# Kernel optimization log

Hardware: AMD Instinct MI355X
Metric: run time of the kernel (lower is better)

Reference implementation:

```python
import jax, jax.numpy as jnp
import numpy as np

N = 8192
ALPHA = 0.1520  # curve_fit of 1/(1+a x^(2b)) to exp(-(x-min_dist)/spread), spread=5, min_dist=1e-5
BETA = 0.7900


def gcn_propagate(x, src, dst, dinv_sqrt):
    # symmetric-normalized aggregation with self loops: A_hat x
    norm = dinv_sqrt[src] * dinv_sqrt[dst]          # [E]
    msg = x[src] * norm[:, None]                     # [E, D]
    agg = jax.ops.segment_sum(msg, dst, num_segments=N)
    agg = agg + x * (dinv_sqrt * dinv_sqrt)[:, None]  # self-loop term x_i / deg_i
    return agg


def setup_inputs() -> dict:
    key = jax.random.key(0)
    k1, k2, k3, k4 = jax.random.split(key, 4)
    E = 262144
    features = jax.random.normal(k1, (N, 512), dtype=jnp.float32)
    edge_index = jax.random.randint(k2, (2, E), 0, N, dtype=jnp.int32)
    W1 = jax.random.normal(k3, (512, 256), dtype=jnp.float32) * 0.05
    b1 = jnp.zeros((256,), dtype=jnp.float32)
    W2 = jax.random.normal(k4, (256, 2), dtype=jnp.float32) * 0.05
    b2 = jnp.zeros((2,), dtype=jnp.float32)
    return {"features": features, "edge_index": edge_index,
            "W1": W1, "b1": b1, "W2": W2, "b2": b2}


def reference(features, edge_index, W1, b1, W2, b2):
    src, dst = edge_index[0], edge_index[1]
    # degree with self loops
    deg = jax.ops.segment_sum(jnp.ones_like(dst, dtype=jnp.float32), dst,
                              num_segments=N) + 1.0
    dinv_sqrt = 1.0 / jnp.sqrt(deg)
    # GCN: layer1 (relu) -> layer2 (linear), dropout_rate=0
    h = gcn_propagate(features, src, dst, dinv_sqrt) @ W1 + b1
    h = jax.nn.relu(h)
    emb = gcn_propagate(h, src, dst, dinv_sqrt) @ W2 + b2   # [N, 2]
    # pairwise squared euclidean distances (cdist^2)
    sq = jnp.sum(emb * emb, axis=1)                          # [N]
    d2 = jnp.maximum(sq[:, None] + sq[None, :] - 2.0 * (emb @ emb.T), 0.0)
    # q = 1 / (1 + alpha * d^(2*beta)) = 1 / (1 + alpha * (d^2)^beta)
    d2_safe = jnp.where(d2 > 0, d2, 1.0)
    pw = jnp.where(d2 > 0, jnp.power(d2_safe, BETA), 0.0)
    q = 1.0 / (1.0 + ALPHA * pw)
    return emb, q
```

## Files before the change

kernel.cpp:

```cpp
#include <hip/hip_runtime.h>
#include <math.h>

#define NN 8192
#define DD 512
#define HH 256
#define EE 262144
#define ALPHAC 0.1520f
#define BETAC  0.7900f

typedef float floatx4 __attribute__((ext_vector_type(4)));

__global__ __launch_bounds__(256) void zero_cnt_kernel(int* __restrict__ cnt) {
  cnt[blockIdx.x * 256 + threadIdx.x] = 0;
}

__global__ __launch_bounds__(256) void count_edges_kernel(const int* __restrict__ dst,
                                                          int* __restrict__ cnt) {
  int e = blockIdx.x * 256 + threadIdx.x;
  atomicAdd(&cnt[dst[e]], 1);
}

__global__ __launch_bounds__(256) void scan_build_kernel(const int* __restrict__ cnt,
    int* __restrict__ row_ptr, int* __restrict__ cursor, float* __restrict__ dinv) {
  int t = threadIdx.x;
  int base = t * 32;
  int local[32];
  int s = 0;
#pragma unroll
  for (int k = 0; k < 32; ++k) { local[k] = cnt[base + k]; s += local[k]; }
  int inc = s;
#pragma unroll
  for (int off = 1; off < 64; off <<= 1) {
    int v = __shfl_up(inc, off, 64);
    if ((t & 63) >= off) inc += v;
  }
  __shared__ int wsum[4];
  int lane = t & 63, wid = t >> 6;
  if (lane == 63) wsum[wid] = inc;
  __syncthreads();
  int woff = 0;
  for (int w = 0; w < wid; ++w) woff += wsum[w];
  int run = woff + inc - s;
#pragma unroll
  for (int k = 0; k < 32; ++k) {
    row_ptr[base + k] = run;
    cursor[base + k] = run;
    dinv[base + k] = rsqrtf((float)cnt[base + k] + 1.0f);
    run += local[k];
  }
  if (t == 255) row_ptr[NN] = run;
}

__global__ __launch_bounds__(256) void scatter_edges_kernel(const int* __restrict__ src,
    const int* __restrict__ dst, int* __restrict__ cursor,
    const float* __restrict__ dinv, int* __restrict__ srcs, float* __restrict__ norms) {
  int e = blockIdx.x * 256 + threadIdx.x;
  int s = src[e], d = dst[e];
  int pos = atomicAdd(&cursor[d], 1);
  srcs[pos] = s;
  norms[pos] = dinv[s];
}

#define BM 128
#define BN 64
#define BK 16
__global__ __launch_bounds__(256) void gemm1_kernel(const float* __restrict__ A,
    const float* __restrict__ B, float* __restrict__ C) {
  __shared__ float As[BK][BM + 4];
  __shared__ float Bs[BK][BN + 4];
  int t = threadIdx.x;
  int tx = t & 15;
  int ty = t >> 4;
  int m0 = blockIdx.y * BM, n0 = blockIdx.x * BN;
  int arow = t >> 1;
  int acol = (t & 1) * 8;
  int brow = t >> 4;
  int bcol = (t & 15) * 4;

  const float* aptr0 = &A[(size_t)(m0 + arow) * DD + acol];
  const float* bptr = &B[(size_t)brow * HH + n0 + bcol];

  float acc[8][4] = {};
  float4 a0v = *(const float4*)(aptr0 + 0);
  float4 a1v = *(const float4*)(aptr0 + 4);
  float4 bv = *(const float4*)(bptr);

  for (int k0 = 0; k0 < DD; k0 += BK) {
    As[acol + 0][arow] = a0v.x; As[acol + 1][arow] = a0v.y;
    As[acol + 2][arow] = a0v.z; As[acol + 3][arow] = a0v.w;
    As[acol + 4][arow] = a1v.x; As[acol + 5][arow] = a1v.y;
    As[acol + 6][arow] = a1v.z; As[acol + 7][arow] = a1v.w;
    *(float4*)&Bs[brow][bcol] = bv;
    __syncthreads();
    if (k0 + BK < DD) {
      a0v = *(const float4*)(aptr0 + k0 + BK + 0);
      a1v = *(const float4*)(aptr0 + k0 + BK + 4);
      bv = *(const float4*)(bptr + (size_t)(k0 + BK) * HH);
    }
#pragma unroll
    for (int k = 0; k < BK; ++k) {
      float4 xa = *(const float4*)&As[k][ty * 8];
      float4 xb = *(const float4*)&As[k][ty * 8 + 4];
      float4 bb = *(const float4*)&Bs[k][tx * 4];
      float am[8] = {xa.x, xa.y, xa.z, xa.w, xb.x, xb.y, xb.z, xb.w};
      float bn[4] = {bb.x, bb.y, bb.z, bb.w};
#pragma unroll
      for (int i = 0; i < 8; ++i)
#pragma unroll
        for (int j = 0; j < 4; ++j) acc[i][j] = fmaf(am[i], bn[j], acc[i][j]);
    }
    __syncthreads();
  }
#pragma unroll
  for (int i = 0; i < 8; ++i) {
    float4 o = make_float4(acc[i][0], acc[i][1], acc[i][2], acc[i][3]);
    *(float4*)&C[(size_t)(m0 + ty * 8 + i) * HH + n0 + tx * 4] = o;
  }
}

__global__ __launch_bounds__(256) void layer1_kernel(const float* __restrict__ t1,
    const int* __restrict__ row_ptr, const int* __restrict__ srcs,
    const float* __restrict__ norms, const float* __restrict__ dinv,
    const float* __restrict__ b1, const float* __restrict__ W2,
    float* __restrict__ t2) {
  int wid = threadIdx.x >> 6;
  int lane = threadIdx.x & 63;
  int i = blockIdx.x * 4 + wid;
  float di = dinv[i];
  int beg = row_ptr[i], end = row_ptr[i + 1];
  float4 acc = make_float4(0.f, 0.f, 0.f, 0.f);
  for (int base = beg; base < end; base += 64) {
    int cnt = end - base;
    if (cnt > 64) cnt = 64;
    int s_reg = 0;
    float n_reg = 0.f;
    if (lane < cnt) { s_reg = srcs[base + lane]; n_reg = norms[base + lane]; }
    int c = 0;
    for (; c + 4 <= cnt; c += 4) {
      int s0 = __shfl(s_reg, c, 64), s1 = __shfl(s_reg, c + 1, 64);
      int s2 = __shfl(s_reg, c + 2, 64), s3 = __shfl(s_reg, c + 3, 64);
      float q0 = __shfl(n_reg, c, 64), q1 = __shfl(n_reg, c + 1, 64);
      float q2 = __shfl(n_reg, c + 2, 64), q3 = __shfl(n_reg, c + 3, 64);
      float4 v0 = *(const float4*)&t1[(size_t)s0 * HH + lane * 4];
      float4 v1 = *(const float4*)&t1[(size_t)s1 * HH + lane * 4];
      float4 v2 = *(const float4*)&t1[(size_t)s2 * HH + lane * 4];
      float4 v3 = *(const float4*)&t1[(size_t)s3 * HH + lane * 4];
      acc.x = fmaf(q0, v0.x, fmaf(q1, v1.x, fmaf(q2, v2.x, fmaf(q3, v3.x, acc.x))));
      acc.y = fmaf(q0, v0.y, fmaf(q1, v1.y, fmaf(q2, v2.y, fmaf(q3, v3.y, acc.y))));
      acc.z = fmaf(q0, v0.z, fmaf(q1, v1.z, fmaf(q2, v2.z, fmaf(q3, v3.z, acc.z))));
      acc.w = fmaf(q0, v0.w, fmaf(q1, v1.w, fmaf(q2, v2.w, fmaf(q3, v3.w, acc.w))));
    }
    for (; c < cnt; ++c) {
      int s = __shfl(s_reg, c, 64);
      float qn = __shfl(n_reg, c, 64);
      float4 v = *(const float4*)&t1[(size_t)s * HH + lane * 4];
      acc.x = fmaf(qn, v.x, acc.x);
      acc.y = fmaf(qn, v.y, acc.y);
      acc.z = fmaf(qn, v.z, acc.z);
      acc.w = fmaf(qn, v.w, acc.w);
    }
  }
  float4 self = *(const float4*)&t1[(size_t)i * HH + lane * 4];
  float4 bv = *(const float4*)&b1[lane * 4];
  float dd = di * di;
  float4 h;
  h.x = fmaxf(fmaf(di, acc.x, fmaf(dd, self.x, bv.x)), 0.f);
  h.y = fmaxf(fmaf(di, acc.y, fmaf(dd, self.y, bv.y)), 0.f);
  h.z = fmaxf(fmaf(di, acc.z, fmaf(dd, self.z, bv.z)), 0.f);
  h.w = fmaxf(fmaf(di, acc.w, fmaf(dd, self.w, bv.w)), 0.f);
  float4 w0 = *(const float4*)&W2[lane * 8];
  float4 w1 = *(const float4*)&W2[lane * 8 + 4];
  float p0 = h.x * w0.x + h.y * w0.z + h.z * w1.x + h.w * w1.z;
  float p1 = h.x * w0.y + h.y * w0.w + h.z * w1.y + h.w * w1.w;
#pragma unroll
  for (int off = 32; off > 0; off >>= 1) {
    p0 += __shfl_down(p0, off, 64);
    p1 += __shfl_down(p1, off, 64);
  }
  if (lane == 0) {
    t2[i * 2 + 0] = p0;
    t2[i * 2 + 1] = p1;
  }
}

__global__ __launch_bounds__(256) void layer2_kernel(const float* __restrict__ t2,
    const int* __restrict__ row_ptr, const int* __restrict__ srcs,
    const float* __restrict__ norms, const float* __restrict__ dinv,
    const float* __restrict__ b2, float* __restrict__ emb, float* __restrict__ sq) {
  int wid = threadIdx.x >> 6;
  int lane = threadIdx.x & 63;
  int i = blockIdx.x * 4 + wid;
  float di = dinv[i];
  int beg = row_ptr[i], end = row_ptr[i + 1];
  float a0 = 0.f, a1 = 0.f;
  for (int e = beg + lane; e < end; e += 64) {
    int s = srcs[e];
    float ns = norms[e];
    a0 += ns * t2[2 * s + 0];
    a1 += ns * t2[2 * s + 1];
  }
#pragma unroll
  for (int off = 32; off > 0; off >>= 1) {
    a0 += __shfl_down(a0, off, 64);
    a1 += __shfl_down(a1, off, 64);
  }
  if (lane == 0) {
    float e0 = di * a0 + di * di * t2[2 * i + 0] + b2[0];
    float e1 = di * a1 + di * di * t2[2 * i + 1] + b2[1];
    emb[2 * i + 0] = e0;
    emb[2 * i + 1] = e1;
    sq[i] = e0 * e0 + e1 * e1;
  }
}

__global__ __launch_bounds__(256) void q_kernel(const float* __restrict__ emb,
    const float* __restrict__ sq, float* __restrict__ q) {
  int t = threadIdx.x;
  int j0 = blockIdx.x * 1024 + t * 4;
  int i0 = blockIdx.y * 32;
  float ex[4], ey[4], sj[4];
#pragma unroll
  for (int jj = 0; jj < 4; ++jj) {
    ex[jj] = emb[2 * (j0 + jj) + 0];
    ey[jj] = emb[2 * (j0 + jj) + 1];
    sj[jj] = sq[j0 + jj];
  }
  for (int ii = 0; ii < 32; ++ii) {
    int i = i0 + ii;
    float xi = emb[2 * i + 0], yi = emb[2 * i + 1], si = sq[i];
    float out4[4];
#pragma unroll
    for (int jj = 0; jj < 4; ++jj) {
      float d2 = si + sj[jj] - 2.f * (xi * ex[jj] + yi * ey[jj]);
      d2 = fmaxf(d2, 0.f);
      float pw = __expf(BETAC * __logf(d2));
      float den = fmaf(ALPHAC, pw, 1.f);
      float qv = __builtin_amdgcn_rcpf(den);
      out4[jj] = (d2 > 0.f) ? qv : 1.f;
    }
    floatx4 r = {out4[0], out4[1], out4[2], out4[3]};
    __builtin_nontemporal_store(r, (floatx4*)&q[(size_t)i * NN + j0]);
  }
}

extern "C" void kernel_launch(void* const* d_in, const int* in_sizes, int n_in,
                              void* d_out, int out_size, void* d_ws, size_t ws_size,
                              hipStream_t stream) {
  const float* features = (const float*)d_in[0];
  const int* edge_index = (const int*)d_in[1];
  const float* W1 = (const float*)d_in[2];
  const float* b1 = (const float*)d_in[3];
  const float* W2 = (const float*)d_in[4];
  const float* b2 = (const float*)d_in[5];
  float* out = (float*)d_out;

  const int* src = edge_index;
  const int* dst = edge_index + EE;

  int* cnt = (int*)d_ws;
  int* row_ptr = cnt + NN;
  int* cursor = row_ptr + 8448;
  int* srcs = cursor + NN;
  float* norms = (float*)(srcs + EE);
  float* dinv = norms + EE;
  float* sqv = dinv + NN;
  float* t2 = sqv + NN;
  float* t1 = t2 + 2 * NN;

  float* emb = out;
  float* qout = out + 2 * NN;

  zero_cnt_kernel<<<NN / 256, 256, 0, stream>>>(cnt);
  count_edges_kernel<<<EE / 256, 256, 0, stream>>>(dst, cnt);
  scan_build_kernel<<<1, 256, 0, stream>>>(cnt, row_ptr, cursor, dinv);
  scatter_edges_kernel<<<EE / 256, 256, 0, stream>>>(src, dst, cursor, dinv, srcs, norms);
  gemm1_kernel<<<dim3(HH / BN, NN / BM), 256, 0, stream>>>(features, W1, t1);
  layer1_kernel<<<NN / 4, 256, 0, stream>>>(t1, row_ptr, srcs, norms, dinv, b1, W2, t2);
  layer2_kernel<<<NN / 4, 256, 0, stream>>>(t2, row_ptr, srcs, norms, dinv, b2, emb, sqv);
  q_kernel<<<dim3(NN / 1024, NN / 32), 256, 0, stream>>>(emb, sqv, qout);
}
```

Measured before the change: 380.7 us.

## Use split-fp16 MFMA for the features×W1 GEMM instead of FP32 FMA

Rewrites gemm1 to split each fp32 input into a high fp16 part and a scaled low fp16 residual. It then runs three 16x16x32 f16 MFMA products per tile (hi*hi, hi*lo, lo*hi) to emulate near-fp32 accuracy on matrix cores. This targets the scalar FMA throughput limit of the old GEMM. The cost is conversion work, extra LDS traffic and 3x the MFMA count, plus a small precision loss from dropping the lo*lo term and fp16 range limits.

```diff
diff --git a/kernel.cpp b/kernel.cpp
--- a/kernel.cpp
+++ b/kernel.cpp
@@ -9,6 +9,8 @@
 #define BETAC  0.7900f
 
 typedef float floatx4 __attribute__((ext_vector_type(4)));
+typedef _Float16 half8 __attribute__((ext_vector_type(8)));
+typedef _Float16 half4 __attribute__((ext_vector_type(4)));
 
 __global__ __launch_bounds__(256) void zero_cnt_kernel(int* __restrict__ cnt) {
   cnt[blockIdx.x * 256 + threadIdx.x] = 0;
@@ -61,61 +63,106 @@
   norms[pos] = dinv[s];
 }
 
-#define BM 128
-#define BN 64
-#define BK 16
+#define LDAH 40
 __global__ __launch_bounds__(256) void gemm1_kernel(const float* __restrict__ A,
     const float* __restrict__ B, float* __restrict__ C) {
-  __shared__ float As[BK][BM + 4];
-  __shared__ float Bs[BK][BN + 4];
+  __shared__ __align__(16) _Float16 AsH[128 * LDAH];
+  __shared__ __align__(16) _Float16 AsL[128 * LDAH];
+  __shared__ __align__(16) _Float16 BtH[64 * LDAH];
+  __shared__ __align__(16) _Float16 BtL[64 * LDAH];
   int t = threadIdx.x;
-  int tx = t & 15;
-  int ty = t >> 4;
-  int m0 = blockIdx.y * BM, n0 = blockIdx.x * BN;
-  int arow = t >> 1;
-  int acol = (t & 1) * 8;
-  int brow = t >> 4;
-  int bcol = (t & 15) * 4;
-
-  const float* aptr0 = &A[(size_t)(m0 + arow) * DD + acol];
-  const float* bptr = &B[(size_t)brow * HH + n0 + bcol];
-
-  float acc[8][4] = {};
-  float4 a0v = *(const float4*)(aptr0 + 0);
-  float4 a1v = *(const float4*)(aptr0 + 4);
-  float4 bv = *(const float4*)(bptr);
-
-  for (int k0 = 0; k0 < DD; k0 += BK) {
-    As[acol + 0][arow] = a0v.x; As[acol + 1][arow] = a0v.y;
-    As[acol + 2][arow] = a0v.z; As[acol + 3][arow] = a0v.w;
-    As[acol + 4][arow] = a1v.x; As[acol + 5][arow] = a1v.y;
-    As[acol + 6][arow] = a1v.z; As[acol + 7][arow] = a1v.w;
-    *(float4*)&Bs[brow][bcol] = bv;
+  int wid = t >> 6, lane = t & 63;
+  int wr = wid >> 1, wc = wid & 1;
+  int m0 = blockIdx.y * 128, n0 = blockIdx.x * 64;
+  int fr = lane & 15;
+  int koff = (lane >> 4) * 8;
+  int bc = t & 63;
+  int bkr = (t >> 6) * 8;
+
+  floatx4 accH[4][2] = {};
+  floatx4 accC[4][2] = {};
+
+  const float* Abase = A + (size_t)m0 * DD;
+  float4 aReg[4];
+  float bReg[8];
+#pragma unroll
+  for (int i = 0; i < 4; ++i) {
+    int f = t + 256 * i;
+    aReg[i] = *(const float4*)&Abase[(size_t)(f >> 3) * DD + (f & 7) * 4];
+  }
+#pragma unroll
+  for (int j = 0; j < 8; ++j) bReg[j] = B[(size_t)(bkr + j) * HH + n0 + bc];
+
+  for (int k0 = 0; k0 < DD; k0 += 32) {
+#pragma unroll
+    for (int i = 0; i < 4; ++i) {
+      int f = t + 256 * i;
+      int row = f >> 3, c4 = f & 7;
+      float4 v = aReg[i];
+      half4 h, l;
+      h.x = (_Float16)v.x; l.x = (_Float16)((v.x - (float)h.x) * 2048.f);
+      h.y = (_Float16)v.y; l.y = (_Float16)((v.y - (float)h.y) * 2048.f);
+      h.z = (_Float16)v.z; l.z = (_Float16)((v.z - (float)h.z) * 2048.f);
+      h.w = (_Float16)v.w; l.w = (_Float16)((v.w - (float)h.w) * 2048.f);
+      *(half4*)&AsH[row * LDAH + c4 * 4] = h;
+      *(half4*)&AsL[row * LDAH + c4 * 4] = l;
+    }
+    {
+      half8 h, l;
+#pragma unroll
+      for (int j = 0; j < 8; ++j) {
+        float v = bReg[j];
+        _Float16 hh = (_Float16)v;
+        h[j] = hh;
+        l[j] = (_Float16)((v - (float)hh) * 2048.f);
+      }
+      *(half8*)&BtH[bc * LDAH + bkr] = h;
+      *(half8*)&BtL[bc * LDAH + bkr] = l;
+    }
     __syncthreads();
-    if (k0 + BK < DD) {
-      a0v = *(const float4*)(aptr0 + k0 + BK + 0);
-      a1v = *(const float4*)(aptr0 + k0 + BK + 4);
-      bv = *(const float4*)(bptr + (size_t)(k0 + BK) * HH);
-    }
-#pragma unroll
-    for (int k = 0; k < BK; ++k) {
-      float4 xa = *(const float4*)&As[k][ty * 8];
-      float4 xb = *(const float4*)&As[k][ty * 8 + 4];
-      float4 bb = *(const float4*)&Bs[k][tx * 4];
-      float am[8] = {xa.x, xa.y, xa.z, xa.w, xb.x, xb.y, xb.z, xb.w};
-      float bn[4] = {bb.x, bb.y, bb.z, bb.w};
-#pragma unroll
-      for (int i = 0; i < 8; ++i)
-#pragma unroll
-        for (int j = 0; j < 4; ++j) acc[i][j] = fmaf(am[i], bn[j], acc[i][j]);
-    }
+    if (k0 + 32 < DD) {
+#pragma unroll
+      for (int i = 0; i < 4; ++i) {
+        int f = t + 256 * i;
+        aReg[i] = *(const float4*)&Abase[(size_t)(f >> 3) * DD + k0 + 32 + (f & 7) * 4];
+      }
+#pragma unroll
+      for (int j = 0; j < 8; ++j) bReg[j] = B[(size_t)(k0 + 32 + bkr + j) * HH + n0 + bc];
+    }
+    half8 aH[4], aL[4], bH[2], bL[2];
+#pragma unroll
+    for (int m = 0; m < 4; ++m) {
+      int r = wr * 64 + m * 16 + fr;
+      aH[m] = *(const half8*)&AsH[r * LDAH + koff];
+      aL[m] = *(const half8*)&AsL[r * LDAH + koff];
+    }
+#pragma unroll
+    for (int n = 0; n < 2; ++n) {
+      int c = wc * 32 + n * 16 + fr;
+      bH[n] = *(const half8*)&BtH[c * LDAH + koff];
+      bL[n] = *(const half8*)&BtL[c * LDAH + koff];
+    }
+#pragma unroll
+    for (int m = 0; m < 4; ++m)
+#pragma unroll
+      for (int n = 0; n < 2; ++n) {
+        accH[m][n] = __builtin_amdgcn_mfma_f32_16x16x32_f16(aH[m], bH[n], accH[m][n], 0, 0, 0);
+        accC[m][n] = __builtin_amdgcn_mfma_f32_16x16x32_f16(aH[m], bL[n], accC[m][n], 0, 0, 0);
+        accC[m][n] = __builtin_amdgcn_mfma_f32_16x16x32_f16(aL[m], bH[n], accC[m][n], 0, 0, 0);
+      }
     __syncthreads();
   }
-#pragma unroll
-  for (int i = 0; i < 8; ++i) {
-    float4 o = make_float4(acc[i][0], acc[i][1], acc[i][2], acc[i][3]);
-    *(float4*)&C[(size_t)(m0 + ty * 8 + i) * HH + n0 + tx * 4] = o;
-  }
+  int orow = m0 + wr * 64 + (lane >> 4) * 4;
+  int ocol = n0 + wc * 32 + (lane & 15);
+#pragma unroll
+  for (int m = 0; m < 4; ++m)
+#pragma unroll
+    for (int n = 0; n < 2; ++n)
+#pragma unroll
+      for (int r = 0; r < 4; ++r) {
+        float v = accH[m][n][r] + accC[m][n][r] * (1.f / 2048.f);
+        C[(size_t)(orow + m * 16 + r) * HH + ocol + n * 16] = v;
+      }
 }
 
 __global__ __launch_bounds__(256) void layer1_kernel(const float* __restrict__ t1,
@@ -274,7 +321,7 @@
   count_edges_kernel<<<EE / 256, 256, 0, stream>>>(dst, cnt);
   scan_build_kernel<<<1, 256, 0, stream>>>(cnt, row_ptr, cursor, dinv);
   scatter_edges_kernel<<<EE / 256, 256, 0, stream>>>(src, dst, cursor, dinv, srcs, norms);
-  gemm1_kernel<<<dim3(HH / BN, NN / BM), 256, 0, stream>>>(features, W1, t1);
+  gemm1_kernel<<<dim3(HH / 64, NN / 128), 256, 0, stream>>>(features, W1, t1);
   layer1_kernel<<<NN / 4, 256, 0, stream>>>(t1, row_ptr, srcs, norms, dinv, b1, W2, t2);
   layer2_kernel<<<NN / 4, 256, 0, stream>>>(t2, row_ptr, srcs, norms, dinv, b2, emb, sqv);
   q_kernel<<<dim3(NN / 1024, NN / 32), 256, 0, stream>>>(emb, sqv, qout);
```

After: 370.0 us. 1.03x faster.
